# Kernel tuning notes

Measured on AMD Instinct MI355X. Metric: run time of the kernel, lower is better.

## Reference

```python
import jax, jax.numpy as jnp
import numpy as np

DIM = 1024
DIM_HEAD = 64
HEADS = 8
INNER = DIM_HEAD * HEADS
EPS = 1e-5


def setup_inputs() -> dict:
    key = jax.random.key(0)
    ks = jax.random.split(key, 5)
    b, n = 4, 2048
    x = jax.random.normal(ks[0], (b, n, DIM), dtype=jnp.float32)
    mask = jnp.ones((b, n), dtype=bool)
    gamma = jnp.ones((DIM,), dtype=jnp.float32)
    null_kv = jax.random.normal(ks[1], (HEADS, 2, DIM_HEAD), dtype=jnp.float32)
    w_qkv = jax.random.normal(ks[2], (DIM, INNER * 3), dtype=jnp.float32) * (DIM ** -0.5)
    w_out = jax.random.normal(ks[3], (INNER, DIM), dtype=jnp.float32) * (INNER ** -0.5)
    return {"x": x, "mask": mask, "gamma": gamma, "null_kv": null_kv,
            "w_qkv": w_qkv, "w_out": w_out}


def _attention(x, mask, gamma, null_kv, w_qkv, w_out):
    b, n, _ = x.shape
    scale = DIM_HEAD ** -0.5
    # RMSNorm (sum-based, as in source): x * rsqrt(sum(x^2) + eps) * gamma * sqrt(dim)
    inv = jax.lax.rsqrt(jnp.sum(x * x, axis=-1, keepdims=True) + EPS)
    xn = x * inv * gamma * (DIM ** 0.5)
    qkv = xn @ w_qkv  # [b, n, 3*inner]
    q, k, v = jnp.split(qkv, 3, axis=-1)
    # b n (h d) -> b h n d
    to_heads = lambda t: t.reshape(b, n, HEADS, DIM_HEAD).transpose(0, 2, 1, 3)
    q, k, v = to_heads(q), to_heads(k), to_heads(v)
    # null kv token prepended along the key axis
    nk = jnp.broadcast_to(null_kv[:, 0][None, :, None, :], (b, HEADS, 1, DIM_HEAD))
    nv = jnp.broadcast_to(null_kv[:, 1][None, :, None, :], (b, HEADS, 1, DIM_HEAD))
    k = jnp.concatenate([nk, k], axis=2)  # [b, h, n+1, d]
    v = jnp.concatenate([nv, v], axis=2)
    q = q * scale
    sim = jnp.einsum('bhid,bhjd->bhij', q, k)  # [b, h, n, n+1]
    max_neg = -jnp.finfo(sim.dtype).max
    # padding mask, padded with True for the null token
    pad_mask = jnp.concatenate([jnp.ones((b, 1), dtype=bool), mask], axis=1)  # [b, n+1]
    sim = jnp.where(pad_mask[:, None, None, :], sim, max_neg)
    # causal mask over the non-null keys; null token (j=0) always visible
    j_idx = jnp.arange(n + 1)
    i_idx = jnp.arange(n)
    causal = (j_idx[None, :] - 1) > i_idx[:, None]  # True where masked
    sim = jnp.where(causal[None, None, :, :], max_neg, sim)
    attn = jax.nn.softmax(sim, axis=-1)
    out = jnp.einsum('bhij,bhjd->bhid', attn, v)  # [b, h, n, d]
    out = out.transpose(0, 2, 1, 3).reshape(b, n, INNER)
    return out @ w_out


def reference(x, mask, gamma, null_kv, w_qkv, w_out):
    return _attention(x, mask, gamma, null_kv, w_qkv, w_out)
```

## Files before the change

### kernel.cpp

```cpp
#include <hip/hip_runtime.h>

typedef unsigned short ushort_t;
typedef __attribute__((ext_vector_type(8))) unsigned short u16x8;
typedef __attribute__((ext_vector_type(4))) unsigned short u16x4;
typedef __attribute__((ext_vector_type(8))) __bf16 bf16x8;
typedef __attribute__((ext_vector_type(4))) float f32x4;

#define NB 4
#define NSEQ 2048
#define NH 8
#define DH 64
#define DMODEL 1024
#define INNERD 512

__device__ inline float b2f(unsigned short s) {
  union { unsigned u; float f; } v; v.u = ((unsigned)s) << 16; return v.f;
}
__device__ inline unsigned short f2b(float f) {
  unsigned u = __float_as_uint(f);
  u += 0x7fffu + ((u >> 16) & 1u);
  return (unsigned short)(u >> 16);
}
__device__ inline float fexp2(float x) {
  float r; asm("v_exp_f32 %0, %1" : "=v"(r) : "v"(x)); return r;
}
__device__ inline f32x4 mfma16(u16x8 a, u16x8 b, f32x4 c) {
  return __builtin_amdgcn_mfma_f32_16x16x32_bf16(
      __builtin_bit_cast(bf16x8, a), __builtin_bit_cast(bf16x8, b), c, 0, 0, 0);
}
__device__ inline void gload_lds16(const ushort_t* g, ushort_t* l) {
  __builtin_amdgcn_global_load_lds(
      (const __attribute__((address_space(1))) void*)g,
      (__attribute__((address_space(3))) void*)l, 16, 0, 0);
}

__global__ __launch_bounds__(256) void transconv_k(const float* __restrict__ in,
                                                   ushort_t* __restrict__ out,
                                                   int R, int C) {
  __shared__ float t[32][33];
  int c0 = blockIdx.x * 32, r0 = blockIdx.y * 32;
  int lx = threadIdx.x & 31, ly = threadIdx.x >> 5;
#pragma unroll
  for (int i = 0; i < 32; i += 8)
    t[ly + i][lx] = in[(size_t)(r0 + ly + i) * C + c0 + lx];
  __syncthreads();
#pragma unroll
  for (int i = 0; i < 32; i += 8)
    out[(size_t)(c0 + ly + i) * R + r0 + lx] = f2b(t[lx][ly + i]);
}

__global__ __launch_bounds__(256) void rmsnorm_k(const float* __restrict__ x,
                                                 const float* __restrict__ g,
                                                 ushort_t* __restrict__ xn) {
  int row = blockIdx.x, tid = threadIdx.x;
  const float* xr = x + (size_t)row * DMODEL;
  float4 v = *(const float4*)(xr + tid * 4);
  float f[4] = {v.x, v.y, v.z, v.w};
  float ss = f[0] * f[0] + f[1] * f[1] + f[2] * f[2] + f[3] * f[3];
#pragma unroll
  for (int d = 32; d; d >>= 1) ss += __shfl_xor(ss, d, 64);
  __shared__ float red[4];
  if ((tid & 63) == 0) red[tid >> 6] = ss;
  __syncthreads();
  float sum = red[0] + red[1] + red[2] + red[3];
  float inv = rsqrtf(sum + 1e-5f) * 32.0f;
  float4 gv = *(const float4*)(g + tid * 4);
  float gg[4] = {gv.x, gv.y, gv.z, gv.w};
  u16x4 o;
#pragma unroll
  for (int i = 0; i < 4; ++i) o[i] = f2b(f[i] * inv * gg[i]);
  *(u16x4*)(xn + (size_t)row * DMODEL + tid * 4) = o;
}

template <int MODE>
__global__ __launch_bounds__(256) void gemm_k(const ushort_t* __restrict__ A,
                                              const ushort_t* __restrict__ Bt,
                                              void* __restrict__ Cv,
                                              void* __restrict__ Kp,
                                              void* __restrict__ Vp,
                                              int M, int Nn, int K, int cpx) {
  int nbx = Nn >> 7;
  int bid = blockIdx.x;
  int swz = (bid & 7) * cpx + (bid >> 3);
  int bn = (swz % nbx) * 128, bm = (swz / nbx) * 128;
  int tid = threadIdx.x;
  int w = tid >> 6, l = tid & 63, lg = l >> 4, lc = l & 15;
  int wm = (w >> 1) * 64, wn = (w & 1) * 64;
  __shared__ __align__(16) ushort_t As[128 * 64];
  __shared__ __align__(16) ushort_t Bs[128 * 64];
  f32x4 acc[4][4];
#pragma unroll
  for (int i = 0; i < 4; ++i)
#pragma unroll
    for (int j = 0; j < 4; ++j) acc[i][j] = (f32x4){0.f, 0.f, 0.f, 0.f};
  int rsub = l >> 3;
  int gsrc = ((l & 7) ^ rsub) * 8;
  for (int k0 = 0; k0 < K; k0 += 64) {
    __syncthreads();
#pragma unroll
    for (int i = 0; i < 4; ++i) {
      int rbase = w * 32 + i * 8;
      gload_lds16(&A[(size_t)(bm + rbase + rsub) * K + k0 + gsrc], &As[rbase * 64]);
      gload_lds16(&Bt[(size_t)(bn + rbase + rsub) * K + k0 + gsrc], &Bs[rbase * 64]);
    }
    __syncthreads();
#pragma unroll
    for (int kk = 0; kk < 2; ++kk) {
      u16x8 af[4], bfr[4];
#pragma unroll
      for (int i = 0; i < 4; ++i) {
        int ra = wm + i * 16 + lc;
        af[i] = *(const u16x8*)&As[ra * 64 + ((kk * 32 + lg * 8) ^ ((ra & 7) * 8))];
        int rb = wn + i * 16 + lc;
        bfr[i] = *(const u16x8*)&Bs[rb * 64 + ((kk * 32 + lg * 8) ^ ((rb & 7) * 8))];
      }
#pragma unroll
      for (int i = 0; i < 4; ++i)
#pragma unroll
        for (int j = 0; j < 4; ++j)
          acc[i][j] = mfma16(af[i], bfr[j], acc[i][j]);
    }
  }
#pragma unroll
  for (int i = 0; i < 4; ++i)
#pragma unroll
    for (int j = 0; j < 4; ++j) {
      int row = bm + wm + i * 16 + lg * 4;
      int cb = bn + wn + j * 16;
      int col = cb + lc;
      if (MODE == 1) {
#pragma unroll
        for (int e = 0; e < 4; ++e)
          ((float*)Cv)[(size_t)(row + e) * Nn + col] = acc[i][j][e];
      } else if (MODE == 0 || cb < 512) {
#pragma unroll
        for (int e = 0; e < 4; ++e)
          ((ushort_t*)Cv)[(size_t)(row + e) * Nn + col] = f2b(acc[i][j][e]);
      } else if (cb < 1024) {
        int h = (cb - 512) >> 6;
        int d = (cb - 512) & 63;
        d += lc;
        int kk = d >> 5, dimgrp = (d >> 3) & 3, j2 = d & 7;
        ushort_t* kt = (ushort_t*)Kp;
#pragma unroll
        for (int e = 0; e < 4; ++e) {
          int n = row + e;
          int b = n >> 11, nn2 = n & 2047;
          int tt = nn2 >> 5, f = (nn2 >> 4) & 1, keylow = nn2 & 15;
          size_t idx = (((size_t)(b * 8 + h) * 64 + tt) * 4 + f * 2 + kk) * 512 +
                       (dimgrp * 16 + keylow) * 8 + j2;
          kt[idx] = f2b(acc[i][j][e]);
        }
      } else {
        int h = (cb - 1024) >> 6;
        int d = (cb - 1024) & 63;
        d += lc;
        int chunk = d >> 4, lcV = d & 15;
        ushort_t* vtl = (ushort_t*)Vp;
#pragma unroll
        for (int e = 0; e < 4; ++e) {
          int n = row + e;
          int b = n >> 11, nn2 = n & 2047;
          int tt = nn2 >> 5, nn = nn2 & 31;
          int j2 = (nn & 3) + ((nn >> 4) << 2);
          int lgv = (nn >> 2) & 3;
          size_t idx = (((size_t)(b * 8 + h) * 64 + tt) * 4 + chunk) * 512 +
                       (lgv * 16 + lcV) * 8 + j2;
          vtl[idx] = f2b(acc[i][j][e]);
        }
      }
    }
}

__global__ __launch_bounds__(256) void attn_k(const ushort_t* __restrict__ qkv,
                                              const ushort_t* __restrict__ kt,
                                              const ushort_t* __restrict__ vtl,
                                              const float* __restrict__ nkv,
                                              ushort_t* __restrict__ aout) {
  int bid = blockIdx.x;
  int tid = threadIdx.x;
  int w = tid >> 6, l = tid & 63, lg = l >> 4, lc = l & 15;
  int s = 63 - (bid >> 5);
  int bh = ((bid & 7) << 2) | ((bid >> 3) & 3);
  int b = bh >> 3, h = bh & 7;
  int i0w = s * 32;

  __shared__ float Om[3][64][17];
  __shared__ float Ml[4][2][2][16];

  const float SCL2 = 0.18033688f;
  const float THR2 = 11.541561f;
  const float M2I = -1.0e30f;
  const float MSK = -3.0e38f;

  u16x8 q[2][2];
#pragma unroll
  for (int qi = 0; qi < 2; ++qi) {
    const ushort_t* qp =
        qkv + (size_t)(b * NSEQ + i0w + qi * 16 + lc) * 1536 + h * 64 + lg * 8;
    q[qi][0] = *(const u16x8*)(qp);
    q[qi][1] = *(const u16x8*)(qp + 32);
  }

  float m2[2], lsum[2];
  f32x4 O[2][4];
  if (w == 0) {
    float nd0 = 0.f, nd1 = 0.f;
#pragma unroll
    for (int kk = 0; kk < 2; ++kk) {
      const float* np = nkv + h * 128 + kk * 32 + lg * 8;
      float4 u = *(const float4*)(np);
      float4 vv = *(const float4*)(np + 4);
      float nk[8] = {u.x, u.y, u.z, u.w, vv.x, vv.y, vv.z, vv.w};
#pragma unroll
      for (int j = 0; j < 8; ++j) {
        nd0 += b2f(q[0][kk][j]) * nk[j];
        nd1 += b2f(q[1][kk][j]) * nk[j];
      }
    }
    nd0 += __shfl_xor(nd0, 16, 64); nd0 += __shfl_xor(nd0, 32, 64);
    nd1 += __shfl_xor(nd1, 16, 64); nd1 += __shfl_xor(nd1, 32, 64);
    m2[0] = nd0 * SCL2; m2[1] = nd1 * SCL2;
    lsum[0] = 0.25f; lsum[1] = 0.25f;
#pragma unroll
    for (int c = 0; c < 4; ++c) {
      float nv = nkv[h * 128 + 64 + c * 16 + lc];
      O[0][c] = (f32x4){nv, nv, nv, nv};
      O[1][c] = (f32x4){nv, nv, nv, nv};
    }
  } else {
    m2[0] = M2I; m2[1] = M2I;
    lsum[0] = 0.f; lsum[1] = 0.f;
#pragma unroll
    for (int c = 0; c < 4; ++c) {
      O[0][c] = (f32x4){0.f, 0.f, 0.f, 0.f};
      O[1][c] = (f32x4){0.f, 0.f, 0.f, 0.f};
    }
  }

  const ushort_t* ktb = kt + ((size_t)bh * 64) * 2048 + l * 8;
  const ushort_t* vtb = vtl + ((size_t)bh * 64) * 2048 + l * 8;

#define LOADK(dst, t_)                                                         \
  do {                                                                         \
    const ushort_t* kp = ktb + (size_t)(t_) * 2048;                            \
    dst[0][0] = *(const u16x8*)(kp);                                           \
    dst[0][1] = *(const u16x8*)(kp + 512);                                     \
    dst[1][0] = *(const u16x8*)(kp + 1024);                                    \
    dst[1][1] = *(const u16x8*)(kp + 1536);                                    \
  } while (0)
#define LOADV(dst, t_)                                                         \
  do {                                                                         \
    const ushort_t* vp = vtb + (size_t)(t_) * 2048;                            \
    dst[0] = *(const u16x8*)(vp);                                              \
    dst[1] = *(const u16x8*)(vp + 512);                                        \
    dst[2] = *(const u16x8*)(vp + 1024);                                       \
    dst[3] = *(const u16x8*)(vp + 1536);                                       \
  } while (0)

  auto body = [&](u16x8(&kf)[2][2], u16x8(&vb)[4], int t, bool last) {
    int k0 = t * 32;
    f32x4 sacc[2][2];
#pragma unroll
    for (int qi = 0; qi < 2; ++qi)
#pragma unroll
      for (int f = 0; f < 2; ++f) {
        sacc[qi][f] = mfma16(kf[f][0], q[qi][0], (f32x4){0.f, 0.f, 0.f, 0.f});
        sacc[qi][f] = mfma16(kf[f][1], q[qi][1], sacc[qi][f]);
      }
    float sv[2][2][4];
    float lmax[2];
#pragma unroll
    for (int qi = 0; qi < 2; ++qi) {
      int qrow = i0w + qi * 16 + lc;
#pragma unroll
      for (int f = 0; f < 2; ++f)
#pragma unroll
        for (int e = 0; e < 4; ++e) {
          float vvv = sacc[qi][f][e] * SCL2;
          if (last && (k0 + f * 16 + lg * 4 + e > qrow)) vvv = MSK;
          sv[qi][f][e] = vvv;
        }
      float a0 = fmaxf(sv[qi][0][0], sv[qi][0][1]);
      float a1 = fmaxf(sv[qi][0][2], sv[qi][0][3]);
      float a2 = fmaxf(sv[qi][1][0], sv[qi][1][1]);
      float a3 = fmaxf(sv[qi][1][2], sv[qi][1][3]);
      lmax[qi] = fmaxf(fmaxf(a0, a1), fmaxf(a2, a3));
    }
    bool need = (lmax[0] > m2[0] + THR2) || (lmax[1] > m2[1] + THR2);
    if (__any(need)) {
#pragma unroll
      for (int qi = 0; qi < 2; ++qi) {
        float mx = fmaxf(lmax[qi], __shfl_xor(lmax[qi], 16, 64));
        mx = fmaxf(mx, __shfl_xor(mx, 32, 64));
        float mn = fmaxf(m2[qi], mx);
        float al = fexp2(m2[qi] - mn);
        m2[qi] = mn;
        lsum[qi] *= al;
        float alr[4];
#pragma unroll
        for (int e = 0; e < 4; ++e) alr[e] = __shfl(al, lg * 4 + e, 64);
#pragma unroll
        for (int c = 0; c < 4; ++c)
#pragma unroll
          for (int e = 0; e < 4; ++e) O[qi][c][e] *= alr[e];
      }
    }
#pragma unroll
    for (int qi = 0; qi < 2; ++qi) {
      float pv[2][4];
#pragma unroll
      for (int f = 0; f < 2; ++f)
#pragma unroll
        for (int e = 0; e < 4; ++e)
          pv[f][e] = fexp2(sv[qi][f][e] - m2[qi]);
      float s0 = (pv[0][0] + pv[0][1]) + (pv[0][2] + pv[0][3]);
      float s1 = (pv[1][0] + pv[1][1]) + (pv[1][2] + pv[1][3]);
      lsum[qi] += s0 + s1;
      union { unsigned u[4]; u16x8 v8; } pa;
      asm("v_cvt_pk_bf16_f32 %0, %1, %2" : "=v"(pa.u[0]) : "v"(pv[0][0]), "v"(pv[0][1]));
      asm("v_cvt_pk_bf16_f32 %0, %1, %2" : "=v"(pa.u[1]) : "v"(pv[0][2]), "v"(pv[0][3]));
      asm("v_cvt_pk_bf16_f32 %0, %1, %2" : "=v"(pa.u[2]) : "v"(pv[1][0]), "v"(pv[1][1]));
      asm("v_cvt_pk_bf16_f32 %0, %1, %2" : "=v"(pa.u[3]) : "v"(pv[1][2]), "v"(pv[1][3]));
#pragma unroll
      for (int c = 0; c < 4; ++c) O[qi][c] = mfma16(pa.v8, vb[c], O[qi][c]);
    }
  };

  u16x8 kfA[2][2], kfB[2][2], vbA[4], vbB[4];
  int t = w;
  if (t <= s) {
    LOADK(kfA, t); LOADV(vbA, t);
    while (true) {
      bool more = (t + 4 <= s);
      if (more) { LOADK(kfB, t + 4); LOADV(vbB, t + 4); }
      body(kfA, vbA, t, t == s);
      if (!more) break;
      t += 4;
      more = (t + 4 <= s);
      if (more) { LOADK(kfA, t + 4); LOADV(vbA, t + 4); }
      body(kfB, vbB, t, t == s);
      if (!more) break;
      t += 4;
    }
  }
#undef LOADK
#undef LOADV

#pragma unroll
  for (int qi = 0; qi < 2; ++qi) {
    lsum[qi] += __shfl_xor(lsum[qi], 16, 64);
    lsum[qi] += __shfl_xor(lsum[qi], 32, 64);
  }
  if (l < 16) {
#pragma unroll
    for (int qi = 0; qi < 2; ++qi) {
      Ml[w][qi][0][lc] = m2[qi];
      Ml[w][qi][1][lc] = lsum[qi];
    }
  }
  for (int qi = 0; qi < 2; ++qi) {
    if (w > 0) {
#pragma unroll
      for (int c = 0; c < 4; ++c)
#pragma unroll
        for (int e = 0; e < 4; ++e) Om[w - 1][l][c * 4 + e] = O[qi][c][e];
    }
    __syncthreads();
    if (w == 0) {
#pragma unroll
      for (int e = 0; e < 4; ++e) {
        int r = lg * 4 + e;
        float mv0 = Ml[0][qi][0][r], mv1 = Ml[1][qi][0][r];
        float mv2 = Ml[2][qi][0][r], mv3 = Ml[3][qi][0][r];
        float mm = fmaxf(fmaxf(mv0, mv1), fmaxf(mv2, mv3));
        float e0 = fexp2(mv0 - mm), e1 = fexp2(mv1 - mm);
        float e2 = fexp2(mv2 - mm), e3 = fexp2(mv3 - mm);
        float ll = e0 * Ml[0][qi][1][r] + e1 * Ml[1][qi][1][r] +
                   e2 * Ml[2][qi][1][r] + e3 * Ml[3][qi][1][r];
        float rl = 1.0f / ll;
        int row = i0w + qi * 16 + r;
        size_t base = (size_t)(b * NSEQ + row) * INNERD + h * 64;
#pragma unroll
        for (int c = 0; c < 4; ++c) {
          int idx = c * 4 + e;
          float o = e0 * O[qi][c][e] + e1 * Om[0][l][idx] +
                    e2 * Om[1][l][idx] + e3 * Om[2][l][idx];
          aout[base + c * 16 + lc] = f2b(o * rl);
        }
      }
    }
    __syncthreads();
  }
}

extern "C" void kernel_launch(void* const* d_in, const int* in_sizes, int n_in,
                              void* d_out, int out_size, void* d_ws, size_t ws_size,
                              hipStream_t stream) {
  (void)in_sizes; (void)n_in; (void)out_size; (void)ws_size;
  const float* x    = (const float*)d_in[0];
  const float* g    = (const float*)d_in[2];
  const float* nkv  = (const float*)d_in[3];
  const float* wqkv = (const float*)d_in[4];
  const float* wout = (const float*)d_in[5];
  float* out = (float*)d_out;
  char* ws = (char*)d_ws;

  ushort_t* xn  = (ushort_t*)(ws);
  ushort_t* qkv = (ushort_t*)(ws + 16777216);
  ushort_t* kt  = (ushort_t*)(ws + 41943040);
  ushort_t* vtl = (ushort_t*)(ws + 50331648);
  ushort_t* wtq = (ushort_t*)(ws + 58720256);
  ushort_t* wto = (ushort_t*)(ws + 61865984);
  ushort_t* ao  = xn;

  transconv_k<<<dim3(1536 / 32, 1024 / 32), 256, 0, stream>>>(wqkv, wtq, 1024, 1536);
  transconv_k<<<dim3(1024 / 32, 512 / 32), 256, 0, stream>>>(wout, wto, 512, 1024);
  rmsnorm_k<<<8192, 256, 0, stream>>>(x, g, xn);
  gemm_k<2><<<768, 256, 0, stream>>>(xn, wtq, qkv, kt, vtl, 8192, 1536, 1024, 96);
  attn_k<<<2048, 256, 0, stream>>>(qkv, kt, vtl, nkv, ao);
  gemm_k<1><<<512, 256, 0, stream>>>(ao, wto, out, nullptr, nullptr, 8192, 1024, 512, 64);
}
```

Measured before the change: 112.5 us.

## Process two key tiles per iteration with restructured K/V prefetch and MFMA priority

Each wave now handles two consecutive 32-key tiles per loop step (64 keys), striding by 8 tiles, instead of one tile striding by 4. This halves the online-softmax rescale checks and max reductions per key. K for the next step is prefetched after the QK MFMAs, while V is loaded at the top of each step instead of double-buffered. s_setprio is raised around the MFMA bursts. It relies on invalid second tiles being masked, and per-wave load balance across the causal diagonal changes. It also risks more exposed V load latency.

Measured after the change: 113.8 us. Within noise of the previous version (+1.1%).

```diff
diff --git a/kernel.cpp b/kernel.cpp
--- a/kernel.cpp
+++ b/kernel.cpp
@@ -241,111 +241,146 @@
   const ushort_t* ktb = kt + ((size_t)bh * 64) * 2048 + l * 8;
   const ushort_t* vtb = vtl + ((size_t)bh * 64) * 2048 + l * 8;
 
-#define LOADK(dst, t_)                                                         \
+#define LOADK2(dst, ta, tb)                                                    \
   do {                                                                         \
-    const ushort_t* kp = ktb + (size_t)(t_) * 2048;                            \
-    dst[0][0] = *(const u16x8*)(kp);                                           \
-    dst[0][1] = *(const u16x8*)(kp + 512);                                     \
-    dst[1][0] = *(const u16x8*)(kp + 1024);                                    \
-    dst[1][1] = *(const u16x8*)(kp + 1536);                                    \
+    const ushort_t* kpa = ktb + (size_t)(ta) * 2048;                           \
+    dst[0][0] = *(const u16x8*)(kpa);                                          \
+    dst[0][1] = *(const u16x8*)(kpa + 512);                                    \
+    dst[1][0] = *(const u16x8*)(kpa + 1024);                                   \
+    dst[1][1] = *(const u16x8*)(kpa + 1536);                                   \
+    const ushort_t* kpb = ktb + (size_t)(tb) * 2048;                           \
+    dst[2][0] = *(const u16x8*)(kpb);                                          \
+    dst[2][1] = *(const u16x8*)(kpb + 512);                                    \
+    dst[3][0] = *(const u16x8*)(kpb + 1024);                                   \
+    dst[3][1] = *(const u16x8*)(kpb + 1536);                                   \
   } while (0)
-#define LOADV(dst, t_)                                                         \
+#define LOADV2(dst, ta, tb)                                                    \
   do {                                                                         \
-    const ushort_t* vp = vtb + (size_t)(t_) * 2048;                            \
-    dst[0] = *(const u16x8*)(vp);                                              \
-    dst[1] = *(const u16x8*)(vp + 512);                                        \
-    dst[2] = *(const u16x8*)(vp + 1024);                                       \
-    dst[3] = *(const u16x8*)(vp + 1536);                                       \
+    const ushort_t* vpa = vtb + (size_t)(ta) * 2048;                           \
+    dst[0] = *(const u16x8*)(vpa);                                             \
+    dst[1] = *(const u16x8*)(vpa + 512);                                       \
+    dst[2] = *(const u16x8*)(vpa + 1024);                                      \
+    dst[3] = *(const u16x8*)(vpa + 1536);                                      \
+    const ushort_t* vpb = vtb + (size_t)(tb) * 2048;                           \
+    dst[4] = *(const u16x8*)(vpb);                                             \
+    dst[5] = *(const u16x8*)(vpb + 512);                                       \
+    dst[6] = *(const u16x8*)(vpb + 1024);                                      \
+    dst[7] = *(const u16x8*)(vpb + 1536);                                      \
   } while (0)
 
-  auto body = [&](u16x8(&kf)[2][2], u16x8(&vb)[4], int t, bool last) {
-    int k0 = t * 32;
-    f32x4 sacc[2][2];
-#pragma unroll
-    for (int qi = 0; qi < 2; ++qi)
-#pragma unroll
-      for (int f = 0; f < 2; ++f) {
-        sacc[qi][f] = mfma16(kf[f][0], q[qi][0], (f32x4){0.f, 0.f, 0.f, 0.f});
-        sacc[qi][f] = mfma16(kf[f][1], q[qi][1], sacc[qi][f]);
-      }
-    float sv[2][2][4];
-    float lmax[2];
-#pragma unroll
-    for (int qi = 0; qi < 2; ++qi) {
-      int qrow = i0w + qi * 16 + lc;
-#pragma unroll
-      for (int f = 0; f < 2; ++f)
-#pragma unroll
-        for (int e = 0; e < 4; ++e) {
-          float vvv = sacc[qi][f][e] * SCL2;
-          if (last && (k0 + f * 16 + lg * 4 + e > qrow)) vvv = MSK;
-          sv[qi][f][e] = vvv;
-        }
-      float a0 = fmaxf(sv[qi][0][0], sv[qi][0][1]);
-      float a1 = fmaxf(sv[qi][0][2], sv[qi][0][3]);
-      float a2 = fmaxf(sv[qi][1][0], sv[qi][1][1]);
-      float a3 = fmaxf(sv[qi][1][2], sv[qi][1][3]);
-      lmax[qi] = fmaxf(fmaxf(a0, a1), fmaxf(a2, a3));
-    }
-    bool need = (lmax[0] > m2[0] + THR2) || (lmax[1] > m2[1] + THR2);
-    if (__any(need)) {
+  u16x8 kf[4][2], vb[8];
+  int t0 = 2 * w;
+  if (t0 <= s) {
+    {
+      int pb = t0 + 1; if (pb > 63) pb = 63;
+      LOADK2(kf, t0, pb);
+    }
+    while (true) {
+      int t1 = t0 + 1;
+      bool v1 = (t1 <= s);
+      int t1c = v1 ? t1 : t0;
+      LOADV2(vb, t0, t1c);
+
+      f32x4 sacc[2][4];
+      __builtin_amdgcn_s_setprio(1);
+#pragma unroll
+      for (int qi = 0; qi < 2; ++qi)
+#pragma unroll
+        for (int f = 0; f < 4; ++f) {
+          sacc[qi][f] = mfma16(kf[f][0], q[qi][0], (f32x4){0.f, 0.f, 0.f, 0.f});
+          sacc[qi][f] = mfma16(kf[f][1], q[qi][1], sacc[qi][f]);
+        }
+      __builtin_amdgcn_s_setprio(0);
+
+      int n0 = t0 + 8;
+      bool more = (n0 <= s);
+      if (more) {
+        int n1 = n0 + 1; if (n1 > 63) n1 = 63;
+        LOADK2(kf, n0, n1);
+      }
+
+      float lmax2[2];
 #pragma unroll
       for (int qi = 0; qi < 2; ++qi) {
-        float mx = fmaxf(lmax[qi], __shfl_xor(lmax[qi], 16, 64));
-        mx = fmaxf(mx, __shfl_xor(mx, 32, 64));
-        float mn = fmaxf(m2[qi], mx);
-        float al = fexp2(m2[qi] - mn);
-        m2[qi] = mn;
-        lsum[qi] *= al;
-        float alr[4];
-#pragma unroll
-        for (int e = 0; e < 4; ++e) alr[e] = __shfl(al, lg * 4 + e, 64);
-#pragma unroll
-        for (int c = 0; c < 4; ++c)
-#pragma unroll
-          for (int e = 0; e < 4; ++e) O[qi][c][e] *= alr[e];
-      }
-    }
-#pragma unroll
-    for (int qi = 0; qi < 2; ++qi) {
-      float pv[2][4];
-#pragma unroll
-      for (int f = 0; f < 2; ++f)
-#pragma unroll
-        for (int e = 0; e < 4; ++e)
-          pv[f][e] = fexp2(sv[qi][f][e] - m2[qi]);
-      float s0 = (pv[0][0] + pv[0][1]) + (pv[0][2] + pv[0][3]);
-      float s1 = (pv[1][0] + pv[1][1]) + (pv[1][2] + pv[1][3]);
-      lsum[qi] += s0 + s1;
-      union { unsigned u[4]; u16x8 v8; } pa;
-      asm("v_cvt_pk_bf16_f32 %0, %1, %2" : "=v"(pa.u[0]) : "v"(pv[0][0]), "v"(pv[0][1]));
-      asm("v_cvt_pk_bf16_f32 %0, %1, %2" : "=v"(pa.u[1]) : "v"(pv[0][2]), "v"(pv[0][3]));
-      asm("v_cvt_pk_bf16_f32 %0, %1, %2" : "=v"(pa.u[2]) : "v"(pv[1][0]), "v"(pv[1][1]));
-      asm("v_cvt_pk_bf16_f32 %0, %1, %2" : "=v"(pa.u[3]) : "v"(pv[1][2]), "v"(pv[1][3]));
-#pragma unroll
-      for (int c = 0; c < 4; ++c) O[qi][c] = mfma16(pa.v8, vb[c], O[qi][c]);
-    }
-  };
-
-  u16x8 kfA[2][2], kfB[2][2], vbA[4], vbB[4];
-  int t = w;
-  if (t <= s) {
-    LOADK(kfA, t); LOADV(vbA, t);
-    while (true) {
-      bool more = (t + 4 <= s);
-      if (more) { LOADK(kfB, t + 4); LOADV(vbB, t + 4); }
-      body(kfA, vbA, t, t == s);
+        int qrow = i0w + qi * 16 + lc;
+#pragma unroll
+        for (int f = 0; f < 4; ++f) {
+          int tt = (f < 2) ? t0 : t1;
+          bool lastf = (tt == s);
+          bool invalid = (f >= 2) && !v1;
+#pragma unroll
+          for (int e = 0; e < 4; ++e) {
+            float vvv = sacc[qi][f][e] * SCL2;
+            if (invalid || (lastf && (tt * 32 + (f & 1) * 16 + lg * 4 + e > qrow)))
+              vvv = MSK;
+            sacc[qi][f][e] = vvv;
+          }
+        }
+        float a0 = fmaxf(fmaxf(sacc[qi][0][0], sacc[qi][0][1]),
+                         fmaxf(sacc[qi][0][2], sacc[qi][0][3]));
+        float a1 = fmaxf(fmaxf(sacc[qi][1][0], sacc[qi][1][1]),
+                         fmaxf(sacc[qi][1][2], sacc[qi][1][3]));
+        float a2 = fmaxf(fmaxf(sacc[qi][2][0], sacc[qi][2][1]),
+                         fmaxf(sacc[qi][2][2], sacc[qi][2][3]));
+        float a3 = fmaxf(fmaxf(sacc[qi][3][0], sacc[qi][3][1]),
+                         fmaxf(sacc[qi][3][2], sacc[qi][3][3]));
+        lmax2[qi] = fmaxf(fmaxf(a0, a1), fmaxf(a2, a3));
+      }
+      bool need = (lmax2[0] > m2[0] + THR2) || (lmax2[1] > m2[1] + THR2);
+      if (__any(need)) {
+#pragma unroll
+        for (int qi = 0; qi < 2; ++qi) {
+          float mx = fmaxf(lmax2[qi], __shfl_xor(lmax2[qi], 16, 64));
+          mx = fmaxf(mx, __shfl_xor(mx, 32, 64));
+          float mn = fmaxf(m2[qi], mx);
+          float al = fexp2(m2[qi] - mn);
+          m2[qi] = mn;
+          lsum[qi] *= al;
+          float alr[4];
+#pragma unroll
+          for (int e = 0; e < 4; ++e) alr[e] = __shfl(al, lg * 4 + e, 64);
+#pragma unroll
+          for (int c = 0; c < 4; ++c)
+#pragma unroll
+            for (int e = 0; e < 4; ++e) O[qi][c][e] *= alr[e];
+        }
+      }
+#pragma unroll
+      for (int qi = 0; qi < 2; ++qi) {
+        float pv[4][4];
+#pragma unroll
+        for (int f = 0; f < 4; ++f)
+#pragma unroll
+          for (int e = 0; e < 4; ++e)
+            pv[f][e] = fexp2(sacc[qi][f][e] - m2[qi]);
+        float s0 = (pv[0][0] + pv[0][1]) + (pv[0][2] + pv[0][3]);
+        float s1 = (pv[1][0] + pv[1][1]) + (pv[1][2] + pv[1][3]);
+        float s2 = (pv[2][0] + pv[2][1]) + (pv[2][2] + pv[2][3]);
+        float s3 = (pv[3][0] + pv[3][1]) + (pv[3][2] + pv[3][3]);
+        lsum[qi] += (s0 + s1) + (s2 + s3);
+        union { unsigned u[4]; u16x8 v8; } pa0, pa1;
+        asm("v_cvt_pk_bf16_f32 %0, %1, %2" : "=v"(pa0.u[0]) : "v"(pv[0][0]), "v"(pv[0][1]));
+        asm("v_cvt_pk_bf16_f32 %0, %1, %2" : "=v"(pa0.u[1]) : "v"(pv[0][2]), "v"(pv[0][3]));
+        asm("v_cvt_pk_bf16_f32 %0, %1, %2" : "=v"(pa0.u[2]) : "v"(pv[1][0]), "v"(pv[1][1]));
+        asm("v_cvt_pk_bf16_f32 %0, %1, %2" : "=v"(pa0.u[3]) : "v"(pv[1][2]), "v"(pv[1][3]));
+        asm("v_cvt_pk_bf16_f32 %0, %1, %2" : "=v"(pa1.u[0]) : "v"(pv[2][0]), "v"(pv[2][1]));
+        asm("v_cvt_pk_bf16_f32 %0, %1, %2" : "=v"(pa1.u[1]) : "v"(pv[2][2]), "v"(pv[2][3]));
+        asm("v_cvt_pk_bf16_f32 %0, %1, %2" : "=v"(pa1.u[2]) : "v"(pv[3][0]), "v"(pv[3][1]));
+        asm("v_cvt_pk_bf16_f32 %0, %1, %2" : "=v"(pa1.u[3]) : "v"(pv[3][2]), "v"(pv[3][3]));
+        __builtin_amdgcn_s_setprio(1);
+#pragma unroll
+        for (int c = 0; c < 4; ++c) {
+          O[qi][c] = mfma16(pa0.v8, vb[c], O[qi][c]);
+          O[qi][c] = mfma16(pa1.v8, vb[4 + c], O[qi][c]);
+        }
+        __builtin_amdgcn_s_setprio(0);
+      }
       if (!more) break;
-      t += 4;
-      more = (t + 4 <= s);
-      if (more) { LOADK(kfA, t + 4); LOADV(vbA, t + 4); }
-      body(kfB, vbB, t, t == s);
-      if (!more) break;
-      t += 4;
-    }
-  }
-#undef LOADK
-#undef LOADV
+      t0 = n0;
+    }
+  }
+#undef LOADK2
+#undef LOADV2
 
 #pragma unroll
   for (int qi = 0; qi < 2; ++qi) {
```
